# Performance work log

Measured on AMD Instinct MI355X. Metric: run time of the kernel, lower is better.

Reference implementation:

```python
import jax, jax.numpy as jnp
import numpy as np

B, C, T = 8, 128, 8192
SIGMA_MIN = 1e-6

def setup_inputs() -> dict:
    key = jax.random.key(0)
    ks = jax.random.split(key, 9)
    x1 = jax.random.normal(ks[0], (B, C, T), dtype=jnp.float32)
    mu = jax.random.normal(ks[1], (B, C, T), dtype=jnp.float32)
    style = jax.random.normal(ks[2], (B, 192), dtype=jnp.float32)
    t_sample = jax.random.uniform(ks[3], (B, 1, 1), dtype=jnp.float32)
    z = jax.random.normal(ks[4], (B, C, T), dtype=jnp.float32)
    W = jax.random.normal(ks[5], (C, C), dtype=jnp.float32) * (1.0 / np.sqrt(C))
    b_lin = jax.random.normal(ks[6], (C,), dtype=jnp.float32) * 0.01
    prompt_lens = jax.random.randint(ks[7], (B,), 64, T // 4)
    x_lens = jax.random.randint(ks[8], (B,), T // 2, T)
    return {"x1": x1, "mu": mu, "style": style, "t_sample": t_sample, "z": z,
            "W": W, "b_lin": b_lin, "x_lens": x_lens, "prompt_lens": prompt_lens}

def reference(x1, mu, style, t_sample, z, W, b_lin, x_lens, prompt_lens):
    # x1, z: [B, C, T]; t_sample: [B, 1, 1]
    sigma = SIGMA_MIN
    Bb, Cc, Tt = x1.shape
    tpos = jnp.arange(Tt)
    pmask = tpos[None, :] < prompt_lens[:, None]            # [B, T] prompt region
    # flow-matching interpolation
    y = (1.0 - (1.0 - sigma) * t_sample) * z + t_sample * x1
    u = x1 - (1.0 - sigma) * z
    # zero out prompt region of y (prompt copy tensor is unused by the mock estimator)
    y = jnp.where(pmask[:, None, :], 0.0, y)
    # mock estimator: per-timestep Linear over channels
    out = jnp.einsum('bct,dc->bdt', y, W) + b_lin[None, :, None]
    # per-sample MSE over [prompt_lens, x_lens) across all channels, then mean over batch
    lmask = (~pmask) & (tpos[None, :] < x_lens[:, None])     # [B, T]
    diff2 = jnp.square(out - u) * lmask[:, None, :]
    counts = (Cc * jnp.sum(lmask, axis=1)).astype(x1.dtype)  # [B]
    loss = jnp.mean(jnp.sum(diff2, axis=(1, 2)) / counts)
    return loss, out + (1.0 - sigma) * z
```

## Files before the change

kernel.cpp:

```cpp
#include <hip/hip_runtime.h>
#include <hip/hip_bf16.h>

#define BB   8
#define CC   128
#define TLEN 8192
#define TT   64
#define TBLK 128
#define NB   (BB * (TLEN / TBLK))

typedef __attribute__((ext_vector_type(8))) short short8;
typedef __attribute__((ext_vector_type(4))) float f32x4;

__device__ __forceinline__ short f2bf(float f) {
    union { float f; unsigned u; } v; v.f = f;
    return (short)((v.u + 0x7FFFu + ((v.u >> 16) & 1u)) >> 16);
}
__device__ __forceinline__ float bf2f(unsigned short h) {
    union { unsigned u; float f; } v; v.u = ((unsigned)h) << 16;
    return v.f;
}
__device__ __forceinline__ int swz(int t, int c) {
    return c ^ (((t ^ (t >> 3)) & 15) << 3);
}
__device__ __forceinline__ void barrier_lds() {
    asm volatile("s_waitcnt lgkmcnt(0)" ::: "memory");
    __builtin_amdgcn_s_barrier();
    asm volatile("" ::: "memory");
}

__device__ __forceinline__ void compute_tile(
    const short (*xb)[CC], const short (*zb)[CC], const short8 (&af)[4],
    int wid, int r15, int q4, int tbase, int b, int pl, int xl,
    float cx, float cz, float oms, const float* __restrict__ blin,
    float* __restrict__ out, float& lsum)
{
    f32x4 aX[4], aZ[4];
    #pragma unroll
    for (int tt = 0; tt < 4; ++tt) { aX[tt] = (f32x4){0,0,0,0}; aZ[tt] = (f32x4){0,0,0,0}; }

    #pragma unroll
    for (int ks = 0; ks < 4; ++ks) {
        #pragma unroll
        for (int tt = 0; tt < 4; ++tt) {
            const int tr = tt * 16 + r15;
            const int cs = swz(tr, ks * 32 + q4 * 8);
            const short8 xa = *reinterpret_cast<const short8*>(&xb[tr][cs]);
            const short8 za = *reinterpret_cast<const short8*>(&zb[tr][cs]);
            aX[tt] = __builtin_amdgcn_mfma_f32_16x16x32_bf16(af[ks], xa, aX[tt], 0, 0, 0);
            aZ[tt] = __builtin_amdgcn_mfma_f32_16x16x32_bf16(af[ks], za, aZ[tt], 0, 0, 0);
        }
    }

    #pragma unroll
    for (int rr = 0; rr < 4; ++rr) {
        const int d  = wid * 16 + q4 * 4 + rr;
        const float bl = blin[d];
        float* orow = out + 1 + (size_t)(b * CC + d) * TLEN + tbase;
        #pragma unroll
        for (int tt = 0; tt < 4; ++tt) {
            const int tl = tt * 16 + r15;
            const int tg = tbase + tl;
            const float s  = cx * aX[tt][rr] + cz * aZ[tt][rr];
            const bool pm  = tg >= pl;
            const float ov = (pm ? s : 0.0f) + bl;
            const int cs   = swz(tl, d);
            const float w  = oms * bf2f((unsigned short)zb[tl][cs]);
            orow[tl] = ov + w;
            if (pm & (tg < xl)) {
                const float xf = bf2f((unsigned short)xb[tl][cs]);
                const float df = ov - (xf - w);
                lsum += df * df;
            }
        }
    }
}

__global__ __launch_bounds__(512, 2)
void cfm_fused(const float* __restrict__ x1, const float* __restrict__ tsm,
               const float* __restrict__ z, const float* __restrict__ W,
               const float* __restrict__ blin, const int* __restrict__ xlens,
               const int* __restrict__ plens, float* __restrict__ out)
{
    __shared__ short xt[2][TT][CC];
    __shared__ short zt[2][TT][CC];
    __shared__ float red[8];

    const int bi = blockIdx.x;
    const int b  = bi & 7;
    const int t0 = (bi >> 3) * TBLK;

    const int tid  = threadIdx.x;
    const int lane = tid & 63;
    const int wid  = tid >> 6;
    const int r15  = lane & 15;
    const int q4   = lane >> 4;

    const float ts  = tsm[b];
    const int   pl  = plens[b];
    const int   xl  = xlens[b];
    const float oms = 0.999999f;
    const float cz  = 1.0f - oms * ts;
    const float cx  = ts;

    const int tj = (tid & 15) * 4;
    const int cr = tid >> 4;
    const size_t gb0 = (size_t)b * CC * TLEN + (size_t)t0 + tj;

    float4 xv0[4], zv0[4];
    #pragma unroll
    for (int p = 0; p < 4; ++p) {
        xv0[p] = *reinterpret_cast<const float4*>(x1 + gb0 + (size_t)(cr + p * 32) * TLEN);
        zv0[p] = *reinterpret_cast<const float4*>(z  + gb0 + (size_t)(cr + p * 32) * TLEN);
    }

    short8 af[4];
    {
        const int row = wid * 16 + r15;
        #pragma unroll
        for (int ks = 0; ks < 4; ++ks) {
            const float4 w0 = *reinterpret_cast<const float4*>(W + row * CC + ks * 32 + q4 * 8);
            const float4 w1 = *reinterpret_cast<const float4*>(W + row * CC + ks * 32 + q4 * 8 + 4);
            short8 a;
            a[0] = f2bf(w0.x); a[1] = f2bf(w0.y); a[2] = f2bf(w0.z); a[3] = f2bf(w0.w);
            a[4] = f2bf(w1.x); a[5] = f2bf(w1.y); a[6] = f2bf(w1.z); a[7] = f2bf(w1.w);
            af[ks] = a;
        }
    }

    #pragma unroll
    for (int p = 0; p < 4; ++p) {
        const int c = cr + p * 32;
        const float* xs = reinterpret_cast<const float*>(&xv0[p]);
        const float* zs = reinterpret_cast<const float*>(&zv0[p]);
        #pragma unroll
        for (int j = 0; j < 4; ++j) {
            const int t  = tj + j;
            const int cs = swz(t, c);
            xt[0][t][cs] = f2bf(xs[j]);
            zt[0][t][cs] = f2bf(zs[j]);
        }
    }

    float4 xv1[4], zv1[4];
    #pragma unroll
    for (int p = 0; p < 4; ++p) {
        xv1[p] = *reinterpret_cast<const float4*>(x1 + gb0 + TT + (size_t)(cr + p * 32) * TLEN);
        zv1[p] = *reinterpret_cast<const float4*>(z  + gb0 + TT + (size_t)(cr + p * 32) * TLEN);
    }

    barrier_lds();

    float lsum = 0.0f;
    compute_tile(xt[0], zt[0], af, wid, r15, q4, t0, b, pl, xl, cx, cz, oms, blin, out, lsum);

    #pragma unroll
    for (int p = 0; p < 4; ++p) {
        const int c = cr + p * 32;
        const float* xs = reinterpret_cast<const float*>(&xv1[p]);
        const float* zs = reinterpret_cast<const float*>(&zv1[p]);
        #pragma unroll
        for (int j = 0; j < 4; ++j) {
            const int t  = tj + j;
            const int cs = swz(t, c);
            xt[1][t][cs] = f2bf(xs[j]);
            zt[1][t][cs] = f2bf(zs[j]);
        }
    }

    barrier_lds();

    compute_tile(xt[1], zt[1], af, wid, r15, q4, t0 + TT, b, pl, xl, cx, cz, oms, blin, out, lsum);

    #pragma unroll
    for (int off = 32; off >= 1; off >>= 1) lsum += __shfl_down(lsum, off);
    if (lane == 0) red[wid] = lsum;
    barrier_lds();
    if (tid == 0) {
        float s = 0.0f;
        #pragma unroll
        for (int w = 0; w < 8; ++w) s += red[w];
        atomicAdd(out, s / (1024.0f * (float)(xl - pl)));
    }
}

extern "C" void kernel_launch(void* const* d_in, const int* in_sizes, int n_in,
                              void* d_out, int out_size, void* d_ws, size_t ws_size,
                              hipStream_t stream) {
    const float* x1    = (const float*)d_in[0];
    const float* tsm   = (const float*)d_in[3];
    const float* z     = (const float*)d_in[4];
    const float* W     = (const float*)d_in[5];
    const float* blin  = (const float*)d_in[6];
    const int*   xlens = (const int*)d_in[7];
    const int*   plens = (const int*)d_in[8];
    float* out = (float*)d_out;

    hipMemsetAsync(out, 0, sizeof(float), stream);
    cfm_fused<<<NB, 512, 0, stream>>>(x1, tsm, z, W, blin, xlens, plens, out);
}
```

Before: 36.27 us.

## Precompute y in staging to halve MFMAs, reload x1 from global for loss

Forms y = cz*z + cx*x1, with the prompt region masked, during LDS staging, so only one MFMA chain over y runs instead of separate chains for x1 and z. The loss now compares the output against x1 re-read from global memory in fp32, rather than the bf16 copy in LDS. The launch-bounds occupancy hint is raised from 2 to 4 blocks per CU. This cuts MFMA work and accumulator registers, but adds a second global read of x1, which should mostly hit in cache.

```diff
diff --git a/kernel.cpp b/kernel.cpp
--- a/kernel.cpp
+++ b/kernel.cpp
@@ -28,15 +28,36 @@
     asm volatile("" ::: "memory");
 }
 
-__device__ __forceinline__ void compute_tile(
-    const short (*xb)[CC], const short (*zb)[CC], const short8 (&af)[4],
+__device__ __forceinline__ void stage_tile(
+    short (*yb)[CC], short (*zb)[CC],
+    const float4 (&xv)[4], const float4 (&zv)[4],
+    int tj, int cr, int tgbase, int pl, float cx, float cz)
+{
+    #pragma unroll
+    for (int p = 0; p < 4; ++p) {
+        const int c = cr + p * 32;
+        const float* xs = reinterpret_cast<const float*>(&xv[p]);
+        const float* zs = reinterpret_cast<const float*>(&zv[p]);
+        #pragma unroll
+        for (int j = 0; j < 4; ++j) {
+            const int t  = tj + j;
+            const int cs = swz(t, c);
+            const float yv = (tgbase + t < pl) ? 0.0f : cz * zs[j] + cx * xs[j];
+            yb[t][cs] = f2bf(yv);
+            zb[t][cs] = f2bf(zs[j]);
+        }
+    }
+}
+
+__device__ __forceinline__ void tile_work(
+    const short (*yb)[CC], const short (*zb)[CC], const short8 (&af)[4],
     int wid, int r15, int q4, int tbase, int b, int pl, int xl,
-    float cx, float cz, float oms, const float* __restrict__ blin,
+    float oms, const float* __restrict__ blin, const float* __restrict__ x1,
     float* __restrict__ out, float& lsum)
 {
-    f32x4 aX[4], aZ[4];
+    f32x4 acc[4];
     #pragma unroll
-    for (int tt = 0; tt < 4; ++tt) { aX[tt] = (f32x4){0,0,0,0}; aZ[tt] = (f32x4){0,0,0,0}; }
+    for (int tt = 0; tt < 4; ++tt) acc[tt] = (f32x4){0.f, 0.f, 0.f, 0.f};
 
     #pragma unroll
     for (int ks = 0; ks < 4; ++ks) {
@@ -44,44 +65,44 @@
         for (int tt = 0; tt < 4; ++tt) {
             const int tr = tt * 16 + r15;
             const int cs = swz(tr, ks * 32 + q4 * 8);
-            const short8 xa = *reinterpret_cast<const short8*>(&xb[tr][cs]);
-            const short8 za = *reinterpret_cast<const short8*>(&zb[tr][cs]);
-            aX[tt] = __builtin_amdgcn_mfma_f32_16x16x32_bf16(af[ks], xa, aX[tt], 0, 0, 0);
-            aZ[tt] = __builtin_amdgcn_mfma_f32_16x16x32_bf16(af[ks], za, aZ[tt], 0, 0, 0);
+            const short8 ya = *reinterpret_cast<const short8*>(&yb[tr][cs]);
+            acc[tt] = __builtin_amdgcn_mfma_f32_16x16x32_bf16(af[ks], ya, acc[tt], 0, 0, 0);
         }
     }
 
     #pragma unroll
     for (int rr = 0; rr < 4; ++rr) {
-        const int d  = wid * 16 + q4 * 4 + rr;
+        const int d   = wid * 16 + q4 * 4 + rr;
         const float bl = blin[d];
-        float* orow = out + 1 + (size_t)(b * CC + d) * TLEN + tbase;
+        const size_t rowoff = (size_t)(b * CC + d) * TLEN + tbase;
+        const float* xrow = x1 + rowoff;
+        float* orow = out + 1 + rowoff;
+        float xg[4];
+        #pragma unroll
+        for (int tt = 0; tt < 4; ++tt) xg[tt] = xrow[tt * 16 + r15];
         #pragma unroll
         for (int tt = 0; tt < 4; ++tt) {
             const int tl = tt * 16 + r15;
             const int tg = tbase + tl;
-            const float s  = cx * aX[tt][rr] + cz * aZ[tt][rr];
-            const bool pm  = tg >= pl;
-            const float ov = (pm ? s : 0.0f) + bl;
-            const int cs   = swz(tl, d);
-            const float w  = oms * bf2f((unsigned short)zb[tl][cs]);
-            orow[tl] = ov + w;
-            if (pm & (tg < xl)) {
-                const float xf = bf2f((unsigned short)xb[tl][cs]);
-                const float df = ov - (xf - w);
+            const float ov = acc[tt][rr] + bl;
+            const float w  = oms * bf2f((unsigned short)zb[tl][swz(tl, d)]);
+            const float o2 = ov + w;
+            orow[tl] = o2;
+            if ((tg >= pl) & (tg < xl)) {
+                const float df = o2 - xg[tt];
                 lsum += df * df;
             }
         }
     }
 }
 
-__global__ __launch_bounds__(512, 2)
+__global__ __launch_bounds__(512, 4)
 void cfm_fused(const float* __restrict__ x1, const float* __restrict__ tsm,
                const float* __restrict__ z, const float* __restrict__ W,
                const float* __restrict__ blin, const int* __restrict__ xlens,
                const int* __restrict__ plens, float* __restrict__ out)
 {
-    __shared__ short xt[2][TT][CC];
+    __shared__ short yt[2][TT][CC];
     __shared__ short zt[2][TT][CC];
     __shared__ float red[8];
 
@@ -112,7 +133,6 @@
         xv0[p] = *reinterpret_cast<const float4*>(x1 + gb0 + (size_t)(cr + p * 32) * TLEN);
         zv0[p] = *reinterpret_cast<const float4*>(z  + gb0 + (size_t)(cr + p * 32) * TLEN);
     }
-
     short8 af[4];
     {
         const int row = wid * 16 + r15;
@@ -126,21 +146,6 @@
             af[ks] = a;
         }
     }
-
-    #pragma unroll
-    for (int p = 0; p < 4; ++p) {
-        const int c = cr + p * 32;
-        const float* xs = reinterpret_cast<const float*>(&xv0[p]);
-        const float* zs = reinterpret_cast<const float*>(&zv0[p]);
-        #pragma unroll
-        for (int j = 0; j < 4; ++j) {
-            const int t  = tj + j;
-            const int cs = swz(t, c);
-            xt[0][t][cs] = f2bf(xs[j]);
-            zt[0][t][cs] = f2bf(zs[j]);
-        }
-    }
-
     float4 xv1[4], zv1[4];
     #pragma unroll
     for (int p = 0; p < 4; ++p) {
@@ -148,28 +153,18 @@
         zv1[p] = *reinterpret_cast<const float4*>(z  + gb0 + TT + (size_t)(cr + p * 32) * TLEN);
     }
 
+    stage_tile(yt[0], zt[0], xv0, zv0, tj, cr, t0, pl, cx, cz);
+
     barrier_lds();
 
     float lsum = 0.0f;
-    compute_tile(xt[0], zt[0], af, wid, r15, q4, t0, b, pl, xl, cx, cz, oms, blin, out, lsum);
+    tile_work(yt[0], zt[0], af, wid, r15, q4, t0, b, pl, xl, oms, blin, x1, out, lsum);
 
-    #pragma unroll
-    for (int p = 0; p < 4; ++p) {
-        const int c = cr + p * 32;
-        const float* xs = reinterpret_cast<const float*>(&xv1[p]);
-        const float* zs = reinterpret_cast<const float*>(&zv1[p]);
-        #pragma unroll
-        for (int j = 0; j < 4; ++j) {
-            const int t  = tj + j;
-            const int cs = swz(t, c);
-            xt[1][t][cs] = f2bf(xs[j]);
-            zt[1][t][cs] = f2bf(zs[j]);
-        }
-    }
+    stage_tile(yt[1], zt[1], xv1, zv1, tj, cr, t0 + TT, pl, cx, cz);
 
     barrier_lds();
 
-    compute_tile(xt[1], zt[1], af, wid, r15, q4, t0 + TT, b, pl, xl, cx, cz, oms, blin, out, lsum);
+    tile_work(yt[1], zt[1], af, wid, r15, q4, t0 + TT, b, pl, xl, oms, blin, x1, out, lsum);
 
     #pragma unroll
     for (int off = 32; off >= 1; off >>= 1) lsum += __shfl_down(lsum, off);
```

Result: slower. 43.06 us (+18.7%).
